# Kernel optimization log

Hardware: AMD Instinct MI355X
Metric: run time of the kernel (lower is better)

The kernel has to match this reference:

```python
import jax, jax.numpy as jnp
import numpy as np

HEAD_NUM = 8
ATT_DIM = 64
NUM_UNITS = HEAD_NUM * ATT_DIM  # 512
B, T, D = 8, 1024, NUM_UNITS
NEG_BIG = -2.0**32 + 1.0


def _sinusoidal_table(max_len, num_hidden):
    P = np.zeros((1, max_len, num_hidden), dtype=np.float32)
    X = np.arange(max_len, dtype=np.float32).reshape(-1, 1) / np.power(
        10000.0, np.arange(0, num_hidden, 2, dtype=np.float32) / num_hidden)
    P[:, :, 0::2] = np.sin(X)
    P[:, :, 1::2] = np.cos(X)
    return P


def setup_inputs() -> dict:
    key = jax.random.key(0)
    ks = jax.random.split(key, 8)
    w_scale = 0.02
    return {
        "queries": jax.random.normal(ks[0], (B, T, D), dtype=jnp.float32),
        "keys": jax.random.normal(ks[1], (B, T, D), dtype=jnp.float32),
        "query_masks": jnp.ones((B, T), dtype=jnp.float32),
        "key_masks": jnp.ones((B, T), dtype=jnp.float32),
        "pos_table": jnp.asarray(_sinusoidal_table(T, D)),
        "W_Query": jax.random.normal(ks[2], (D, D), dtype=jnp.float32) * w_scale,
        "W_key": jax.random.normal(ks[3], (D, D), dtype=jnp.float32) * w_scale,
        "W_Value": jax.random.normal(ks[4], (D, D), dtype=jnp.float32) * w_scale,
        "fw1": jax.random.normal(ks[5], (D, 4 * D), dtype=jnp.float32) * w_scale,
        "fw2": jax.random.normal(ks[6], (4 * D, D), dtype=jnp.float32) * w_scale,
    }


def reference(queries, keys, query_masks, key_masks, pos_table,
              W_Query, W_key, W_Value, fw1, fw2):
    h, dh = HEAD_NUM, ATT_DIM
    pe_scale = jnp.asarray(NUM_UNITS ** 0.5, dtype=queries.dtype)
    pos = pos_table[:, :queries.shape[1], :] * pe_scale  # scale=True
    q_in = queries + pos
    k_in = keys + pos

    q = jnp.einsum('btd,de->bte', q_in, W_Query)
    k = jnp.einsum('btd,de->bte', k_in, W_key)
    # Faithful to source: values computed from the projected keys.
    v = jnp.einsum('btd,de->bte', k, W_Value)

    # split heads: (B,T,h*dh) -> (h,B,T,dh)
    def heads(x):
        return x.reshape(B, T, h, dh).transpose(2, 0, 1, 3)
    qh, kh, vh = heads(q), heads(k), heads(v)

    scores = jnp.einsum('hbqd,hbkd->hbqk', qh, kh) / (dh ** 0.5)
    # key padding mask
    scores = jnp.where(key_masks[None, :, None, :] == 1.0, scores, NEG_BIG)
    # blinding: mask the diagonal
    eye = jnp.eye(T, dtype=bool)
    scores = jnp.where(eye[None, None, :, :], NEG_BIG, scores)
    attn = jax.nn.softmax(scores, axis=-1)
    attn = attn * query_masks[None, :, :, None]

    out = jnp.einsum('hbqk,hbkd->hbqd', attn, vh)
    result = out.transpose(1, 2, 0, 3).reshape(B, T, D)  # merge heads

    result = result + q_in  # residual (use_res, queries after PE)

    # feed-forward with residual
    hidden = jax.nn.relu(jnp.einsum('btd,df->btf', result, fw1))
    ffn = jnp.einsum('btf,fd->btd', hidden, fw2)
    result = result + ffn

    # output_type == 'mean'
    return jnp.mean(result, axis=1, keepdims=True)  # (B,1,D)
```

## Files before the change

### kernel.cpp

```cpp
#include <hip/hip_runtime.h>


typedef __bf16 bf16x8 __attribute__((ext_vector_type(8)));
typedef __bf16 bf16x4 __attribute__((ext_vector_type(4)));
typedef float f32x4 __attribute__((ext_vector_type(4)));
typedef unsigned short u16x8 __attribute__((ext_vector_type(8)));
typedef unsigned short u16x4 __attribute__((ext_vector_type(4)));

#define MFMA_BF16(a, b, c) __builtin_amdgcn_mfma_f32_16x16x32_bf16((a), (b), (c), 0, 0, 0)
#define NEGBIG (-4294967295.0f)
#define QSCALE 0.18033688011112042f
#define EXP2(x) __builtin_amdgcn_exp2f(x)

#define GLL16(g, l)                                                                 \
    __builtin_amdgcn_global_load_lds((__attribute__((address_space(1))) void*)(g),  \
                                     (__attribute__((address_space(3))) void*)(l),  \
                                     16, 0, 0)

static __device__ __forceinline__ unsigned short f2bf(float f) {
    __bf16 h = (__bf16)f;
    return __builtin_bit_cast(unsigned short, h);
}
static __device__ __forceinline__ float bf2f(unsigned short h) {
    return __builtin_bit_cast(float, ((unsigned int)h) << 16);
}

__global__ __launch_bounds__(256) void prep_kernel(
    const float* __restrict__ q, const float* __restrict__ k,
    const float* __restrict__ pos,
    unsigned short* __restrict__ qo, unsigned short* __restrict__ ko)
{
    size_t i = ((size_t)blockIdx.x * 256 + threadIdx.x) * 4;
    size_t td = i & (size_t)(1024 * 512 - 1);
    float4 qv = *(const float4*)(q + i);
    float4 kv = *(const float4*)(k + i);
    float4 pv = *(const float4*)(pos + td);
    const float S = 22.627416997969522f;
    u16x4 qr, kr;
    qr[0] = f2bf(qv.x + pv.x * S); qr[1] = f2bf(qv.y + pv.y * S);
    qr[2] = f2bf(qv.z + pv.z * S); qr[3] = f2bf(qv.w + pv.w * S);
    kr[0] = f2bf(kv.x + pv.x * S); kr[1] = f2bf(kv.y + pv.y * S);
    kr[2] = f2bf(kv.z + pv.z * S); kr[3] = f2bf(kv.w + pv.w * S);
    *(u16x4*)(qo + i) = qr;
    *(u16x4*)(ko + i) = kr;
}

__global__ __launch_bounds__(256) void wconv_kernel(
    const float* __restrict__ w0, const float* __restrict__ w1, const float* __restrict__ w2,
    const float* __restrict__ w3, const float* __restrict__ w4,
    unsigned short* __restrict__ o0, unsigned short* __restrict__ o1, unsigned short* __restrict__ o2,
    unsigned short* __restrict__ o3, unsigned short* __restrict__ o4,
    unsigned short* __restrict__ wkp)
{
    int id = blockIdx.x;
    const float* in; unsigned short* out; int K, N, kt, nt; bool dup = false;
    if (id < 768) {
        int m = id >> 8; id &= 255;
        in  = (m == 0) ? w0 : ((m == 1) ? w1 : w2);
        out = (m == 0) ? o0 : ((m == 1) ? o1 : o2);
        dup = (m == 1);
        K = 512; N = 512; kt = id >> 4; nt = id & 15;
    } else if (id < 1792) {
        id -= 768; in = w3; out = o3; K = 512; N = 2048; kt = id >> 6; nt = id & 63;
    } else {
        id -= 1792; in = w4; out = o4; K = 2048; N = 512; kt = id >> 4; nt = id & 15;
    }
    int k0 = kt * 32, n0 = nt * 32;
    __shared__ float tile[32][33];
    int tx = threadIdx.x & 31, ty = threadIdx.x >> 5;
#pragma unroll
    for (int i = 0; i < 32; i += 8) {
        float v = in[(size_t)(k0 + ty + i) * N + n0 + tx];
        tile[ty + i][tx] = v;
        if (dup) wkp[(size_t)(k0 + ty + i) * 512 + n0 + tx] = f2bf(v);
    }
    __syncthreads();
#pragma unroll
    for (int i = 0; i < 32; i += 8)
        out[(size_t)(n0 + ty + i) * K + k0 + tx] = f2bf(tile[tx][ty + i]);
}

__global__ __launch_bounds__(256) void gemm64(
    const unsigned short* __restrict__ A, const unsigned short* __restrict__ Bt,
    unsigned short* __restrict__ C, int N, int K)
{
    __shared__ unsigned short As[64 * 32];
    __shared__ unsigned short Bs[64 * 32];
    const int tid = threadIdx.x;
    const int wave = tid >> 6, lane = tid & 63;
    const int g = lane >> 4, lr = lane & 15;
    const int wm = (wave >> 1) * 32, wn = (wave & 1) * 32;
    const size_t bm = (size_t)blockIdx.x * 64, bn = (size_t)blockIdx.y * 64;
    const int row = tid >> 2, kc = (tid & 3) * 8;
    const unsigned short* Ap = A + (bm + row) * (size_t)K + kc;
    const unsigned short* Bp = Bt + (bn + row) * (size_t)K + kc;
    unsigned short* AsW = As + tid * 8;
    unsigned short* BsW = Bs + tid * 8;

    f32x4 acc[2][2] = {};
    for (int k0 = 0; k0 < K; k0 += 32) {
        __syncthreads();
        GLL16(Ap + k0, AsW);
        GLL16(Bp + k0, BsW);
        __syncthreads();
        bf16x8 af[2], bfr[2];
#pragma unroll
        for (int t = 0; t < 2; ++t) {
            af[t]  = *(const bf16x8*)&As[(wm + t * 16 + lr) * 32 + g * 8];
            bfr[t] = *(const bf16x8*)&Bs[(wn + t * 16 + lr) * 32 + g * 8];
        }
#pragma unroll
        for (int i = 0; i < 2; ++i)
#pragma unroll
            for (int j = 0; j < 2; ++j)
                acc[i][j] = MFMA_BF16(af[i], bfr[j], acc[i][j]);
    }
#pragma unroll
    for (int i = 0; i < 2; ++i)
#pragma unroll
        for (int j = 0; j < 2; ++j) {
            size_t rr = bm + wm + i * 16 + g * 4;
            size_t cc = bn + wn + j * 16 + lr;
#pragma unroll
            for (int r = 0; r < 4; ++r)
                C[(rr + r) * (size_t)N + cc] = f2bf(acc[i][j][r]);
        }
}

static __device__ __forceinline__ void gemm_core(
    const unsigned short* __restrict__ A,
    const unsigned short* __restrict__ Bt,
    unsigned short* __restrict__ C,
    int N, int K, int mode,
    unsigned short* As, unsigned short* Bs, int bx, int by)
{
    const int tid = threadIdx.x;
    const int wave = tid >> 6, lane = tid & 63;
    const int g = lane >> 4, lr = lane & 15;
    const int wm = (wave >> 1) * 64, wn = (wave & 1) * 64;
    const size_t bm = (size_t)bx * 128, bn = (size_t)by * 128;

    const int srow = tid >> 2, skc = (tid & 3) * 8;
    const unsigned short* Ap = A + (bm + srow) * (size_t)K + skc;
    const unsigned short* Bp = Bt + (bn + srow) * (size_t)K + skc;
    unsigned short* AsW = As + tid * 8;
    unsigned short* BsW = Bs + tid * 8;

    f32x4 acc[4][4] = {};
    for (int k0 = 0; k0 < K; k0 += 32) {
        __syncthreads();
        GLL16(Ap + k0, AsW);
        GLL16(Ap + (size_t)64 * K + k0, AsW + 2048);
        GLL16(Bp + k0, BsW);
        GLL16(Bp + (size_t)64 * K + k0, BsW + 2048);
        __syncthreads();
        bf16x8 af[4], bfr[4];
#pragma unroll
        for (int t = 0; t < 4; ++t) {
            af[t]  = *(const bf16x8*)&As[(wm + t * 16 + lr) * 32 + g * 8];
            bfr[t] = *(const bf16x8*)&Bs[(wn + t * 16 + lr) * 32 + g * 8];
        }
#pragma unroll
        for (int rt = 0; rt < 4; ++rt)
#pragma unroll
            for (int ct = 0; ct < 4; ++ct)
                acc[rt][ct] = MFMA_BF16(af[rt], bfr[ct], acc[rt][ct]);
    }

#pragma unroll
    for (int rt = 0; rt < 4; ++rt)
#pragma unroll
        for (int ct = 0; ct < 4; ++ct) {
            size_t row = bm + wm + rt * 16 + g * 4;
            size_t col = bn + wn + ct * 16 + lr;
#pragma unroll
            for (int r = 0; r < 4; ++r) {
                float x = acc[rt][ct][r];
                if (mode == 2) x *= QSCALE;
                C[(row + r) * (size_t)N + col] = f2bf(x);
            }
        }
}

__global__ __launch_bounds__(256, 2) void proj3_kernel(
    const unsigned short* __restrict__ q_in, const unsigned short* __restrict__ k_in,
    const unsigned short* __restrict__ wqt, const unsigned short* __restrict__ wkt,
    const unsigned short* __restrict__ wkvt,
    unsigned short* __restrict__ qb, unsigned short* __restrict__ kb,
    unsigned short* __restrict__ vb)
{
    __shared__ unsigned short As[128 * 32];
    __shared__ unsigned short Bs[128 * 32];
    const unsigned short *A, *Bt; unsigned short* C; int mode = 0;
    switch (blockIdx.z) {
        case 0:  A = q_in; Bt = wqt;  C = qb; mode = 2; break;
        case 1:  A = k_in; Bt = wkt;  C = kb; break;
        default: A = k_in; Bt = wkvt; C = vb; break;
    }
    gemm_core(A, Bt, C, 512, 512, mode, As, Bs, blockIdx.x, blockIdx.y);
}

__global__ __launch_bounds__(256, 2) void ffn1_mean(
    const unsigned short* __restrict__ A,
    const unsigned short* __restrict__ Bt,
    float* __restrict__ hmean)
{
    __shared__ unsigned short As[128 * 32];
    __shared__ unsigned short Bs[128 * 32];
    const int tid = threadIdx.x;
    const int wave = tid >> 6, lane = tid & 63;
    const int g = lane >> 4, lr = lane & 15;
    const int wm = (wave >> 1) * 64, wn = (wave & 1) * 64;
    const size_t bm = (size_t)blockIdx.x * 128, bn = (size_t)blockIdx.y * 128;

    const int srow = tid >> 2, skc = (tid & 3) * 8;
    const unsigned short* Ap = A + (bm + srow) * (size_t)512 + skc;
    const unsigned short* Bp = Bt + (bn + srow) * (size_t)512 + skc;
    unsigned short* AsW = As + tid * 8;
    unsigned short* BsW = Bs + tid * 8;

    f32x4 acc[4][4] = {};
    for (int k0 = 0; k0 < 512; k0 += 32) {
        __syncthreads();
        GLL16(Ap + k0, AsW);
        GLL16(Ap + (size_t)64 * 512 + k0, AsW + 2048);
        GLL16(Bp + k0, BsW);
        GLL16(Bp + (size_t)64 * 512 + k0, BsW + 2048);
        __syncthreads();
        bf16x8 af[4], bfr[4];
#pragma unroll
        for (int t = 0; t < 4; ++t) {
            af[t]  = *(const bf16x8*)&As[(wm + t * 16 + lr) * 32 + g * 8];
            bfr[t] = *(const bf16x8*)&Bs[(wn + t * 16 + lr) * 32 + g * 8];
        }
#pragma unroll
        for (int rt = 0; rt < 4; ++rt)
#pragma unroll
            for (int ct = 0; ct < 4; ++ct)
                acc[rt][ct] = MFMA_BF16(af[rt], bfr[ct], acc[rt][ct]);
    }

    const int b = blockIdx.x >> 3;
#pragma unroll
    for (int ct = 0; ct < 4; ++ct) {
        float s = 0.f;
#pragma unroll
        for (int rt = 0; rt < 4; ++rt)
#pragma unroll
            for (int r = 0; r < 4; ++r) s += fmaxf(acc[rt][ct][r], 0.f);
        s += __shfl_xor(s, 16, 64);
        s += __shfl_xor(s, 32, 64);
        if (g == 0)
            atomicAdd(hmean + b * 2048 + bn + wn + ct * 16 + lr, s);
    }
}

__global__ __launch_bounds__(256) void ffn2_small(
    const float* __restrict__ hmean, const unsigned short* __restrict__ fw2t,
    float* __restrict__ out)
{
    __shared__ float red[256];
    const int b = blockIdx.x;
    const int d = blockIdx.y * 64 + (threadIdx.x & 63);
    const int fs = (threadIdx.x >> 6) * 512;
    const float* hm = hmean + b * 2048 + fs;
    const unsigned short* wr = fw2t + (size_t)d * 2048 + fs;
    float acc = 0.f;
    for (int f = 0; f < 512; f += 8) {
        u16x8 w = *(const u16x8*)(wr + f);
        f32x4 h0 = *(const f32x4*)(hm + f);
        f32x4 h1 = *(const f32x4*)(hm + f + 4);
        acc += h0[0] * bf2f(w[0]) + h0[1] * bf2f(w[1]) + h0[2] * bf2f(w[2]) + h0[3] * bf2f(w[3])
             + h1[0] * bf2f(w[4]) + h1[1] * bf2f(w[5]) + h1[2] * bf2f(w[6]) + h1[3] * bf2f(w[7]);
    }
    red[threadIdx.x] = acc;
    __syncthreads();
    if (threadIdx.x < 64) {
        float s = red[threadIdx.x] + red[threadIdx.x + 64] +
                  red[threadIdx.x + 128] + red[threadIdx.x + 192];
        out[b * 512 + d] += s * (1.0f / 1024.0f);
    }
}

__global__ __launch_bounds__(512, 2) void attn_kernel(
    const unsigned short* __restrict__ Q,
    const unsigned short* __restrict__ Kp,
    const unsigned short* __restrict__ V,
    const float* __restrict__ queries,
    const float* __restrict__ pos,
    const float* __restrict__ kmask,
    const float* __restrict__ qmask,
    unsigned short* __restrict__ Res,
    float* __restrict__ out)
{
    __shared__ unsigned short Ks[2][64 * 72];
    __shared__ unsigned short Vts[2][64 * 72];
    __shared__ unsigned short Ps[8][16 * 72];
    __shared__ float kbias[1024];
    const int tid = threadIdx.x, wave = tid >> 6, lane = tid & 63;
    const int g = lane >> 4, lr = lane & 15;
    const int b = blockIdx.y >> 3, h = blockIdx.y & 7;
    const int qg = blockIdx.x * 128 + wave * 16 + lr;

    for (int i = tid; i < 1024; i += 512)
        kbias[i] = (kmask[b * 1024 + i] == 1.0f) ? 0.f : NEGBIG;

    bf16x8 aq0, aq1;
    {
        const unsigned short* qp = Q + ((size_t)(b * 1024 + qg)) * 512 + h * 64 + g * 8;
        aq0 = *(const bf16x8*)qp;
        aq1 = *(const bf16x8*)(qp + 32);
    }
    const float qm = qmask[b * 1024 + qg];

    float m_run = -3.0e38f, l_run = 0.f;
    f32x4 o[4] = {};

    const unsigned short* kbase = Kp + ((size_t)(b * 1024)) * 512 + h * 64;
    const unsigned short* vbase = V + ((size_t)(b * 1024)) * 512 + h * 64;

    const int half = tid >> 8;
    const int skey = (tid & 255) >> 2, sd = (tid & 3) * 16;
    const int vk0 = (tid & 15) * 4, vd0 = ((tid >> 4) & 15) * 4;

    u16x8 kr0, kr1; u16x4 vr[4];
    if (half) {
        const unsigned short* kp = kbase + (size_t)skey * 512 + sd;
        kr0 = *(const u16x8*)kp; kr1 = *(const u16x8*)(kp + 8);
    } else {
        const unsigned short* vp = vbase + (size_t)vk0 * 512 + vd0;
#pragma unroll
        for (int j = 0; j < 4; ++j) vr[j] = *(const u16x4*)(vp + (size_t)j * 512);
    }
    if (half) {
        *(u16x8*)&Ks[0][skey * 72 + sd] = kr0;
        *(u16x8*)&Ks[0][skey * 72 + sd + 8] = kr1;
    } else {
#pragma unroll
        for (int i = 0; i < 4; ++i) {
            u16x4 w = { vr[0][i], vr[1][i], vr[2][i], vr[3][i] };
            *(u16x4*)&Vts[0][(vd0 + i) * 72 + vk0] = w;
        }
    }
    if (half) {
        const unsigned short* kp = kbase + (size_t)(64 + skey) * 512 + sd;
        kr0 = *(const u16x8*)kp; kr1 = *(const u16x8*)(kp + 8);
    } else {
        const unsigned short* vp = vbase + (size_t)(64 + vk0) * 512 + vd0;
#pragma unroll
        for (int j = 0; j < 4; ++j) vr[j] = *(const u16x4*)(vp + (size_t)j * 512);
    }
    __syncthreads();

    for (int it = 0; it < 16; ++it) {
        const int j0 = it * 64;
        const unsigned short* Kc = Ks[it & 1];
        const unsigned short* Vc = Vts[it & 1];

        f32x4 s[4];
#pragma unroll
        for (int ct = 0; ct < 4; ++ct) {
            bf16x8 ka = *(const bf16x8*)&Kc[(ct * 16 + lr) * 72 + g * 8];
            bf16x8 kc = *(const bf16x8*)&Kc[(ct * 16 + lr) * 72 + 32 + g * 8];
            f32x4 z = {};
            z = MFMA_BF16(ka, aq0, z);
            s[ct] = MFMA_BF16(kc, aq1, z);
        }

#pragma unroll
        for (int ct = 0; ct < 4; ++ct)
            s[ct] += *(const f32x4*)&kbias[j0 + ct * 16 + g * 4];
        if (((qg ^ j0) & ~63) == 0) {
#pragma unroll
            for (int ct = 0; ct < 4; ++ct) {
                unsigned diff = (unsigned)(qg - (j0 + ct * 16 + g * 4));
                if (diff < 4u) s[ct][diff] = NEGBIG;
            }
        }
        float rmax = -3.0e38f;
#pragma unroll
        for (int ct = 0; ct < 4; ++ct)
#pragma unroll
            for (int r = 0; r < 4; ++r) rmax = fmaxf(rmax, s[ct][r]);
        rmax = fmaxf(rmax, __shfl_xor(rmax, 16, 64));
        rmax = fmaxf(rmax, __shfl_xor(rmax, 32, 64));

        float mn = fmaxf(m_run, rmax);
        float alpha = EXP2(m_run - mn);
        m_run = mn;
        float psum = 0.f;
#pragma unroll
        for (int ct = 0; ct < 4; ++ct) {
            f32x4 p;
#pragma unroll
            for (int r = 0; r < 4; ++r) { p[r] = EXP2(s[ct][r] - mn); psum += p[r]; }
            bf16x4 pk = { (__bf16)p[0], (__bf16)p[1], (__bf16)p[2], (__bf16)p[3] };
            *(bf16x4*)&Ps[wave][lr * 72 + ct * 16 + g * 4] = pk;
        }
        psum += __shfl_xor(psum, 16, 64);
        psum += __shfl_xor(psum, 32, 64);
        l_run = l_run * alpha + psum;
#pragma unroll
        for (int dt = 0; dt < 4; ++dt) o[dt] *= alpha;

        bf16x8 p0 = *(const bf16x8*)&Ps[wave][lr * 72 + g * 8];
        bf16x8 p1 = *(const bf16x8*)&Ps[wave][lr * 72 + 32 + g * 8];
#pragma unroll
        for (int dt = 0; dt < 4; ++dt) {
            bf16x8 va = *(const bf16x8*)&Vc[(dt * 16 + lr) * 72 + g * 8];
            bf16x8 vc = *(const bf16x8*)&Vc[(dt * 16 + lr) * 72 + 32 + g * 8];
            o[dt] = MFMA_BF16(va, p0, o[dt]);
            o[dt] = MFMA_BF16(vc, p1, o[dt]);
        }

        if (it + 1 < 16) {
            unsigned short* Kn = Ks[(it + 1) & 1];
            unsigned short* Vn = Vts[(it + 1) & 1];
            if (half) {
                *(u16x8*)&Kn[skey * 72 + sd] = kr0;
                *(u16x8*)&Kn[skey * 72 + sd + 8] = kr1;
            } else {
#pragma unroll
                for (int i = 0; i < 4; ++i) {
                    u16x4 w = { vr[0][i], vr[1][i], vr[2][i], vr[3][i] };
                    *(u16x4*)&Vn[(vd0 + i) * 72 + vk0] = w;
                }
            }
        }
        if (it + 2 < 16) {
            const int jn = (it + 2) * 64;
            if (half) {
                const unsigned short* kp = kbase + (size_t)(jn + skey) * 512 + sd;
                kr0 = *(const u16x8*)kp; kr1 = *(const u16x8*)(kp + 8);
            } else {
                const unsigned short* vp = vbase + (size_t)(jn + vk0) * 512 + vd0;
#pragma unroll
                for (int j = 0; j < 4; ++j) vr[j] = *(const u16x4*)(vp + (size_t)j * 512);
            }
        }
        __syncthreads();
    }

    const float inv_l = 1.0f / l_run;
    const float S = 22.627416997969522f;
    float vals[4][4];
#pragma unroll
    for (int dt = 0; dt < 4; ++dt) {
        size_t col = (size_t)h * 64 + dt * 16 + g * 4;
        size_t idx = ((size_t)(b * 1024 + qg)) * 512 + col;
        f32x4 qv = *(const f32x4*)&queries[idx];
        f32x4 pv = *(const f32x4*)&pos[(size_t)qg * 512 + col];
        u16x4 wr;
#pragma unroll
        for (int r = 0; r < 4; ++r) {
            float v = o[dt][r] * inv_l * qm + qv[r] + pv[r] * S;
            vals[dt][r] = v;
            wr[r] = f2bf(v);
        }
        *(u16x4*)&Res[idx] = wr;
    }

    float* red = kbias;
#pragma unroll
    for (int dt = 0; dt < 4; ++dt)
#pragma unroll
        for (int r = 0; r < 4; ++r) {
            float x = vals[dt][r];
            x += __shfl_xor(x, 1, 64);
            x += __shfl_xor(x, 2, 64);
            x += __shfl_xor(x, 4, 64);
            x += __shfl_xor(x, 8, 64);
            if (lr == 0) red[wave * 64 + dt * 16 + g * 4 + r] = x;
        }
    __syncthreads();
    if (tid < 64) {
        float s = 0.f;
#pragma unroll
        for (int w = 0; w < 8; ++w) s += red[w * 64 + tid];
        atomicAdd(out + b * 512 + h * 64 + tid, s * (1.0f / 1024.0f));
    }
}

extern "C" void kernel_launch(void* const* d_in, const int* in_sizes, int n_in,
                              void* d_out, int out_size, void* d_ws, size_t ws_size,
                              hipStream_t stream)
{
    (void)in_sizes; (void)n_in; (void)out_size; (void)ws_size;
    const float* queries     = (const float*)d_in[0];
    const float* keys        = (const float*)d_in[1];
    const float* query_masks = (const float*)d_in[2];
    const float* key_masks   = (const float*)d_in[3];
    const float* pos_table   = (const float*)d_in[4];
    const float* W_Query     = (const float*)d_in[5];
    const float* W_key       = (const float*)d_in[6];
    const float* W_Value     = (const float*)d_in[7];
    const float* fw1         = (const float*)d_in[8];
    const float* fw2         = (const float*)d_in[9];
    float* out = (float*)d_out;

    unsigned short* ws = (unsigned short*)d_ws;
    const size_t NE = (size_t)8 * 1024 * 512;
    unsigned short* q_in   = ws;
    unsigned short* k_in   = ws + NE;
    unsigned short* qb     = ws + 2 * NE;
    unsigned short* kb     = ws + 3 * NE;
    unsigned short* vb     = ws + 4 * NE;
    unsigned short* result = q_in;
    unsigned short* wqt    = ws + 6 * NE;
    unsigned short* wkt    = wqt + 512 * 512;
    unsigned short* wvt    = wkt + 512 * 512;
    unsigned short* fw1t   = wvt + 512 * 512;
    unsigned short* fw2t   = fw1t + 2048 * 512;
    unsigned short* wkp    = fw2t + 2048 * 512;
    unsigned short* wkvt   = wkp + 512 * 512;
    float*          hmean  = (float*)(wkvt + 512 * 512);

    hipMemsetAsync(d_out, 0, 8 * 512 * sizeof(float), stream);
    hipMemsetAsync(hmean, 0, 8 * 2048 * sizeof(float), stream);
    prep_kernel<<<4096, 256, 0, stream>>>(queries, keys, pos_table, q_in, k_in);
    wconv_kernel<<<2816, 256, 0, stream>>>(W_Query, W_key, W_Value, fw1, fw2,
                                           wqt, wkt, wvt, fw1t, fw2t, wkp);
    gemm64<<<dim3(8, 8), 256, 0, stream>>>(wvt, wkp, wkvt, 512, 512);
    proj3_kernel<<<dim3(64, 4, 3), 256, 0, stream>>>(q_in, k_in, wqt, wkt, wkvt, qb, kb, vb);
    attn_kernel<<<dim3(8, 64), 512, 0, stream>>>(qb, kb, vb, queries, pos_table,
                                                 key_masks, query_masks, result, out);
    ffn1_mean<<<dim3(64, 16), 256, 0, stream>>>(result, fw1t, hmean);
    ffn2_small<<<dim3(8, 8), 256, 0, stream>>>(hmean, fw2t, out);
}
```

Measured before the change: 212.4 us.

## Deepen GEMM K-tile to 64 and process 128 keys per attention step

The projection and FFN1 GEMMs now stage a 64-wide K slice per iteration, which halves the number of barrier pairs at the cost of doubled LDS per block. The attention kernel swaps double-buffered 64-key tiles for 128-key steps with register prefetch, so each softmax rescale covers twice the keys and there are fewer iterations. This adds a second barrier per step and the prefetch no longer overlaps the LDS stores. The attention grid is also transposed so consecutive blocks cover different batch/head pairs.

```diff
diff --git a/kernel.cpp b/kernel.cpp
--- a/kernel.cpp
+++ b/kernel.cpp
@@ -143,28 +143,33 @@
     const int srow = tid >> 2, skc = (tid & 3) * 8;
     const unsigned short* Ap = A + (bm + srow) * (size_t)K + skc;
     const unsigned short* Bp = Bt + (bn + srow) * (size_t)K + skc;
-    unsigned short* AsW = As + tid * 8;
-    unsigned short* BsW = Bs + tid * 8;
 
     f32x4 acc[4][4] = {};
-    for (int k0 = 0; k0 < K; k0 += 32) {
-        __syncthreads();
-        GLL16(Ap + k0, AsW);
-        GLL16(Ap + (size_t)64 * K + k0, AsW + 2048);
-        GLL16(Bp + k0, BsW);
-        GLL16(Bp + (size_t)64 * K + k0, BsW + 2048);
-        __syncthreads();
-        bf16x8 af[4], bfr[4];
-#pragma unroll
-        for (int t = 0; t < 4; ++t) {
-            af[t]  = *(const bf16x8*)&As[(wm + t * 16 + lr) * 32 + g * 8];
-            bfr[t] = *(const bf16x8*)&Bs[(wn + t * 16 + lr) * 32 + g * 8];
-        }
-#pragma unroll
-        for (int rt = 0; rt < 4; ++rt)
-#pragma unroll
-            for (int ct = 0; ct < 4; ++ct)
-                acc[rt][ct] = MFMA_BF16(af[rt], bfr[ct], acc[rt][ct]);
+    for (int k0 = 0; k0 < K; k0 += 64) {
+        __syncthreads();
+        GLL16(Ap + k0,                        As + tid * 8);
+        GLL16(Ap + (size_t)64 * K + k0,       As + 2048 + tid * 8);
+        GLL16(Ap + k0 + 32,                   As + 4096 + tid * 8);
+        GLL16(Ap + (size_t)64 * K + k0 + 32,  As + 6144 + tid * 8);
+        GLL16(Bp + k0,                        Bs + tid * 8);
+        GLL16(Bp + (size_t)64 * K + k0,       Bs + 2048 + tid * 8);
+        GLL16(Bp + k0 + 32,                   Bs + 4096 + tid * 8);
+        GLL16(Bp + (size_t)64 * K + k0 + 32,  Bs + 6144 + tid * 8);
+        __syncthreads();
+#pragma unroll
+        for (int kk = 0; kk < 2; ++kk) {
+            bf16x8 af[4], bfr[4];
+#pragma unroll
+            for (int t = 0; t < 4; ++t) {
+                af[t]  = *(const bf16x8*)&As[kk * 4096 + (wm + t * 16 + lr) * 32 + g * 8];
+                bfr[t] = *(const bf16x8*)&Bs[kk * 4096 + (wn + t * 16 + lr) * 32 + g * 8];
+            }
+#pragma unroll
+            for (int rt = 0; rt < 4; ++rt)
+#pragma unroll
+                for (int ct = 0; ct < 4; ++ct)
+                    acc[rt][ct] = MFMA_BF16(af[rt], bfr[ct], acc[rt][ct]);
+        }
     }
 
 #pragma unroll
@@ -189,8 +194,8 @@
     unsigned short* __restrict__ qb, unsigned short* __restrict__ kb,
     unsigned short* __restrict__ vb)
 {
-    __shared__ unsigned short As[128 * 32];
-    __shared__ unsigned short Bs[128 * 32];
+    __shared__ unsigned short As[128 * 64];
+    __shared__ unsigned short Bs[128 * 64];
     const unsigned short *A, *Bt; unsigned short* C; int mode = 0;
     switch (blockIdx.z) {
         case 0:  A = q_in; Bt = wqt;  C = qb; mode = 2; break;
@@ -205,8 +210,8 @@
     const unsigned short* __restrict__ Bt,
     float* __restrict__ hmean)
 {
-    __shared__ unsigned short As[128 * 32];
-    __shared__ unsigned short Bs[128 * 32];
+    __shared__ unsigned short As[128 * 64];
+    __shared__ unsigned short Bs[128 * 64];
     const int tid = threadIdx.x;
     const int wave = tid >> 6, lane = tid & 63;
     const int g = lane >> 4, lr = lane & 15;
@@ -216,28 +221,33 @@
     const int srow = tid >> 2, skc = (tid & 3) * 8;
     const unsigned short* Ap = A + (bm + srow) * (size_t)512 + skc;
     const unsigned short* Bp = Bt + (bn + srow) * (size_t)512 + skc;
-    unsigned short* AsW = As + tid * 8;
-    unsigned short* BsW = Bs + tid * 8;
 
     f32x4 acc[4][4] = {};
-    for (int k0 = 0; k0 < 512; k0 += 32) {
-        __syncthreads();
-        GLL16(Ap + k0, AsW);
-        GLL16(Ap + (size_t)64 * 512 + k0, AsW + 2048);
-        GLL16(Bp + k0, BsW);
-        GLL16(Bp + (size_t)64 * 512 + k0, BsW + 2048);
-        __syncthreads();
-        bf16x8 af[4], bfr[4];
-#pragma unroll
-        for (int t = 0; t < 4; ++t) {
-            af[t]  = *(const bf16x8*)&As[(wm + t * 16 + lr) * 32 + g * 8];
-            bfr[t] = *(const bf16x8*)&Bs[(wn + t * 16 + lr) * 32 + g * 8];
-        }
-#pragma unroll
-        for (int rt = 0; rt < 4; ++rt)
-#pragma unroll
-            for (int ct = 0; ct < 4; ++ct)
-                acc[rt][ct] = MFMA_BF16(af[rt], bfr[ct], acc[rt][ct]);
+    for (int k0 = 0; k0 < 512; k0 += 64) {
+        __syncthreads();
+        GLL16(Ap + k0,                         As + tid * 8);
+        GLL16(Ap + (size_t)64 * 512 + k0,      As + 2048 + tid * 8);
+        GLL16(Ap + k0 + 32,                    As + 4096 + tid * 8);
+        GLL16(Ap + (size_t)64 * 512 + k0 + 32, As + 6144 + tid * 8);
+        GLL16(Bp + k0,                         Bs + tid * 8);
+        GLL16(Bp + (size_t)64 * 512 + k0,      Bs + 2048 + tid * 8);
+        GLL16(Bp + k0 + 32,                    Bs + 4096 + tid * 8);
+        GLL16(Bp + (size_t)64 * 512 + k0 + 32, Bs + 6144 + tid * 8);
+        __syncthreads();
+#pragma unroll
+        for (int kk = 0; kk < 2; ++kk) {
+            bf16x8 af[4], bfr[4];
+#pragma unroll
+            for (int t = 0; t < 4; ++t) {
+                af[t]  = *(const bf16x8*)&As[kk * 4096 + (wm + t * 16 + lr) * 32 + g * 8];
+                bfr[t] = *(const bf16x8*)&Bs[kk * 4096 + (wn + t * 16 + lr) * 32 + g * 8];
+            }
+#pragma unroll
+            for (int rt = 0; rt < 4; ++rt)
+#pragma unroll
+                for (int ct = 0; ct < 4; ++ct)
+                    acc[rt][ct] = MFMA_BF16(af[rt], bfr[ct], acc[rt][ct]);
+        }
     }
 
     const int b = blockIdx.x >> 3;
@@ -295,12 +305,12 @@
 {
     __shared__ unsigned short Ks[2][64 * 72];
     __shared__ unsigned short Vts[2][64 * 72];
-    __shared__ unsigned short Ps[8][16 * 72];
+    __shared__ unsigned short Ps[8][16 * 152];
     __shared__ float kbias[1024];
     const int tid = threadIdx.x, wave = tid >> 6, lane = tid & 63;
     const int g = lane >> 4, lr = lane & 15;
-    const int b = blockIdx.y >> 3, h = blockIdx.y & 7;
-    const int qg = blockIdx.x * 128 + wave * 16 + lr;
+    const int b = blockIdx.x >> 3, h = blockIdx.x & 7;
+    const int qg = blockIdx.y * 128 + wave * 16 + lr;
 
     for (int i = tid; i < 1024; i += 512)
         kbias[i] = (kmask[b * 1024 + i] == 1.0f) ? 0.f : NEGBIG;
@@ -323,65 +333,93 @@
     const int skey = (tid & 255) >> 2, sd = (tid & 3) * 16;
     const int vk0 = (tid & 15) * 4, vd0 = ((tid >> 4) & 15) * 4;
 
-    u16x8 kr0, kr1; u16x4 vr[4];
+    u16x8 kr[2][2]; u16x4 vr[2][4];
     if (half) {
-        const unsigned short* kp = kbase + (size_t)skey * 512 + sd;
-        kr0 = *(const u16x8*)kp; kr1 = *(const u16x8*)(kp + 8);
+#pragma unroll
+        for (int pt = 0; pt < 2; ++pt) {
+            const unsigned short* kp = kbase + (size_t)(pt * 64 + skey) * 512 + sd;
+            kr[pt][0] = *(const u16x8*)kp; kr[pt][1] = *(const u16x8*)(kp + 8);
+        }
     } else {
-        const unsigned short* vp = vbase + (size_t)vk0 * 512 + vd0;
-#pragma unroll
-        for (int j = 0; j < 4; ++j) vr[j] = *(const u16x4*)(vp + (size_t)j * 512);
-    }
-    if (half) {
-        *(u16x8*)&Ks[0][skey * 72 + sd] = kr0;
-        *(u16x8*)&Ks[0][skey * 72 + sd + 8] = kr1;
-    } else {
-#pragma unroll
-        for (int i = 0; i < 4; ++i) {
-            u16x4 w = { vr[0][i], vr[1][i], vr[2][i], vr[3][i] };
-            *(u16x4*)&Vts[0][(vd0 + i) * 72 + vk0] = w;
-        }
-    }
-    if (half) {
-        const unsigned short* kp = kbase + (size_t)(64 + skey) * 512 + sd;
-        kr0 = *(const u16x8*)kp; kr1 = *(const u16x8*)(kp + 8);
-    } else {
-        const unsigned short* vp = vbase + (size_t)(64 + vk0) * 512 + vd0;
-#pragma unroll
-        for (int j = 0; j < 4; ++j) vr[j] = *(const u16x4*)(vp + (size_t)j * 512);
-    }
-    __syncthreads();
-
-    for (int it = 0; it < 16; ++it) {
-        const int j0 = it * 64;
-        const unsigned short* Kc = Ks[it & 1];
-        const unsigned short* Vc = Vts[it & 1];
-
-        f32x4 s[4];
-#pragma unroll
-        for (int ct = 0; ct < 4; ++ct) {
-            bf16x8 ka = *(const bf16x8*)&Kc[(ct * 16 + lr) * 72 + g * 8];
-            bf16x8 kc = *(const bf16x8*)&Kc[(ct * 16 + lr) * 72 + 32 + g * 8];
-            f32x4 z = {};
-            z = MFMA_BF16(ka, aq0, z);
-            s[ct] = MFMA_BF16(kc, aq1, z);
-        }
-
-#pragma unroll
-        for (int ct = 0; ct < 4; ++ct)
-            s[ct] += *(const f32x4*)&kbias[j0 + ct * 16 + g * 4];
-        if (((qg ^ j0) & ~63) == 0) {
+#pragma unroll
+        for (int pt = 0; pt < 2; ++pt) {
+            const unsigned short* vp = vbase + (size_t)(pt * 64 + vk0) * 512 + vd0;
+#pragma unroll
+            for (int j = 0; j < 4; ++j) vr[pt][j] = *(const u16x4*)(vp + (size_t)j * 512);
+        }
+    }
+
+    for (int it = 0; it < 8; ++it) {
+        __syncthreads();
+        if (half) {
+#pragma unroll
+            for (int pt = 0; pt < 2; ++pt) {
+                *(u16x8*)&Ks[pt][skey * 72 + sd] = kr[pt][0];
+                *(u16x8*)&Ks[pt][skey * 72 + sd + 8] = kr[pt][1];
+            }
+        } else {
+#pragma unroll
+            for (int pt = 0; pt < 2; ++pt)
+#pragma unroll
+                for (int i = 0; i < 4; ++i) {
+                    u16x4 w = { vr[pt][0][i], vr[pt][1][i], vr[pt][2][i], vr[pt][3][i] };
+                    *(u16x4*)&Vts[pt][(vd0 + i) * 72 + vk0] = w;
+                }
+        }
+        __syncthreads();
+        if (it < 7) {
+            const int jn = (it + 1) * 128;
+            if (half) {
+#pragma unroll
+                for (int pt = 0; pt < 2; ++pt) {
+                    const unsigned short* kp = kbase + (size_t)(jn + pt * 64 + skey) * 512 + sd;
+                    kr[pt][0] = *(const u16x8*)kp; kr[pt][1] = *(const u16x8*)(kp + 8);
+                }
+            } else {
+#pragma unroll
+                for (int pt = 0; pt < 2; ++pt) {
+                    const unsigned short* vp = vbase + (size_t)(jn + pt * 64 + vk0) * 512 + vd0;
+#pragma unroll
+                    for (int j = 0; j < 4; ++j) vr[pt][j] = *(const u16x4*)(vp + (size_t)j * 512);
+                }
+            }
+        }
+
+        const int j0 = it * 128;
+        f32x4 s[2][4];
+#pragma unroll
+        for (int pt = 0; pt < 2; ++pt)
 #pragma unroll
             for (int ct = 0; ct < 4; ++ct) {
-                unsigned diff = (unsigned)(qg - (j0 + ct * 16 + g * 4));
-                if (diff < 4u) s[ct][diff] = NEGBIG;
-            }
-        }
+                bf16x8 ka = *(const bf16x8*)&Ks[pt][(ct * 16 + lr) * 72 + g * 8];
+                bf16x8 kc = *(const bf16x8*)&Ks[pt][(ct * 16 + lr) * 72 + 32 + g * 8];
+                f32x4 z = {};
+                z = MFMA_BF16(ka, aq0, z);
+                s[pt][ct] = MFMA_BF16(kc, aq1, z);
+            }
+
+#pragma unroll
+        for (int pt = 0; pt < 2; ++pt)
+#pragma unroll
+            for (int ct = 0; ct < 4; ++ct)
+                s[pt][ct] += *(const f32x4*)&kbias[j0 + pt * 64 + ct * 16 + g * 4];
+#pragma unroll
+        for (int pt = 0; pt < 2; ++pt)
+            if (((qg ^ (j0 + pt * 64)) & ~63) == 0) {
+#pragma unroll
+                for (int ct = 0; ct < 4; ++ct) {
+                    unsigned diff = (unsigned)(qg - (j0 + pt * 64 + ct * 16 + g * 4));
+                    if (diff < 4u) s[pt][ct][diff] = NEGBIG;
+                }
+            }
+
         float rmax = -3.0e38f;
 #pragma unroll
-        for (int ct = 0; ct < 4; ++ct)
-#pragma unroll
-            for (int r = 0; r < 4; ++r) rmax = fmaxf(rmax, s[ct][r]);
+        for (int pt = 0; pt < 2; ++pt)
+#pragma unroll
+            for (int ct = 0; ct < 4; ++ct)
+#pragma unroll
+                for (int r = 0; r < 4; ++r) rmax = fmaxf(rmax, s[pt][ct][r]);
         rmax = fmaxf(rmax, __shfl_xor(rmax, 16, 64));
         rmax = fmaxf(rmax, __shfl_xor(rmax, 32, 64));
 
@@ -390,55 +428,33 @@
         m_run = mn;
         float psum = 0.f;
 #pragma unroll
-        for (int ct = 0; ct < 4; ++ct) {
-            f32x4 p;
-#pragma unroll
-            for (int r = 0; r < 4; ++r) { p[r] = EXP2(s[ct][r] - mn); psum += p[r]; }
-            bf16x4 pk = { (__bf16)p[0], (__bf16)p[1], (__bf16)p[2], (__bf16)p[3] };
-            *(bf16x4*)&Ps[wave][lr * 72 + ct * 16 + g * 4] = pk;
-        }
+        for (int pt = 0; pt < 2; ++pt)
+#pragma unroll
+            for (int ct = 0; ct < 4; ++ct) {
+                f32x4 p;
+#pragma unroll
+                for (int r = 0; r < 4; ++r) { p[r] = EXP2(s[pt][ct][r] - mn); psum += p[r]; }
+                bf16x4 pk = { (__bf16)p[0], (__bf16)p[1], (__bf16)p[2], (__bf16)p[3] };
+                *(bf16x4*)&Ps[wave][lr * 152 + pt * 64 + ct * 16 + g * 4] = pk;
+            }
         psum += __shfl_xor(psum, 16, 64);
         psum += __shfl_xor(psum, 32, 64);
         l_run = l_run * alpha + psum;
 #pragma unroll
         for (int dt = 0; dt < 4; ++dt) o[dt] *= alpha;
 
-        bf16x8 p0 = *(const bf16x8*)&Ps[wave][lr * 72 + g * 8];
-        bf16x8 p1 = *(const bf16x8*)&Ps[wave][lr * 72 + 32 + g * 8];
-#pragma unroll
-        for (int dt = 0; dt < 4; ++dt) {
-            bf16x8 va = *(const bf16x8*)&Vc[(dt * 16 + lr) * 72 + g * 8];
-            bf16x8 vc = *(const bf16x8*)&Vc[(dt * 16 + lr) * 72 + 32 + g * 8];
-            o[dt] = MFMA_BF16(va, p0, o[dt]);
-            o[dt] = MFMA_BF16(vc, p1, o[dt]);
-        }
-
-        if (it + 1 < 16) {
-            unsigned short* Kn = Ks[(it + 1) & 1];
-            unsigned short* Vn = Vts[(it + 1) & 1];
-            if (half) {
-                *(u16x8*)&Kn[skey * 72 + sd] = kr0;
-                *(u16x8*)&Kn[skey * 72 + sd + 8] = kr1;
-            } else {
-#pragma unroll
-                for (int i = 0; i < 4; ++i) {
-                    u16x4 w = { vr[0][i], vr[1][i], vr[2][i], vr[3][i] };
-                    *(u16x4*)&Vn[(vd0 + i) * 72 + vk0] = w;
-                }
-            }
-        }
-        if (it + 2 < 16) {
-            const int jn = (it + 2) * 64;
-            if (half) {
-                const unsigned short* kp = kbase + (size_t)(jn + skey) * 512 + sd;
-                kr0 = *(const u16x8*)kp; kr1 = *(const u16x8*)(kp + 8);
-            } else {
-                const unsigned short* vp = vbase + (size_t)(jn + vk0) * 512 + vd0;
-#pragma unroll
-                for (int j = 0; j < 4; ++j) vr[j] = *(const u16x4*)(vp + (size_t)j * 512);
-            }
-        }
-        __syncthreads();
+#pragma unroll
+        for (int pt = 0; pt < 2; ++pt) {
+            bf16x8 p0 = *(const bf16x8*)&Ps[wave][lr * 152 + pt * 64 + g * 8];
+            bf16x8 p1 = *(const bf16x8*)&Ps[wave][lr * 152 + pt * 64 + 32 + g * 8];
+#pragma unroll
+            for (int dt = 0; dt < 4; ++dt) {
+                bf16x8 va = *(const bf16x8*)&Vts[pt][(dt * 16 + lr) * 72 + g * 8];
+                bf16x8 vc = *(const bf16x8*)&Vts[pt][(dt * 16 + lr) * 72 + 32 + g * 8];
+                o[dt] = MFMA_BF16(va, p0, o[dt]);
+                o[dt] = MFMA_BF16(vc, p1, o[dt]);
+            }
+        }
     }
 
     const float inv_l = 1.0f / l_run;
@@ -522,7 +538,7 @@
                                            wqt, wkt, wvt, fw1t, fw2t, wkp);
     gemm64<<<dim3(8, 8), 256, 0, stream>>>(wvt, wkp, wkvt, 512, 512);
     proj3_kernel<<<dim3(64, 4, 3), 256, 0, stream>>>(q_in, k_in, wqt, wkt, wkvt, qb, kb, vb);
-    attn_kernel<<<dim3(8, 64), 512, 0, stream>>>(qb, kb, vb, queries, pos_table,
+    attn_kernel<<<dim3(64, 8), 512, 0, stream>>>(qb, kb, vb, queries, pos_table,
                                                  key_masks, query_masks, result, out);
     ffn1_mean<<<dim3(64, 16), 256, 0, stream>>>(result, fw1t, hmean);
     ffn2_small<<<dim3(8, 8), 256, 0, stream>>>(hmean, fw2t, out);
```

New measurement: 223.1 us. 1.05x slower.
